# Performance work log

Measured on AMD Instinct MI355X. Metric: run time of the kernel, lower is better.

The kernel has to match this reference:

```python
import jax, jax.numpy as jnp
import numpy as np

B, S, D, F, E, K = 4, 1024, 512, 1024, 8, 2
LB_W, Z_W = 0.01, 0.001

def setup_inputs() -> dict:
    key = jax.random.key(0)
    k1, k2, k3, k4, k5 = jax.random.split(key, 5)
    std = 0.02
    x = jax.random.normal(k1, (B, S, D), dtype=jnp.float32)
    router_w = jax.random.normal(k2, (E, D), dtype=jnp.float32) * std  # nn.Linear weight [out,in]
    gate_w = jax.random.normal(k3, (E, D, F), dtype=jnp.float32) * std
    up_w = jax.random.normal(k4, (E, D, F), dtype=jnp.float32) * std
    down_w = jax.random.normal(k5, (E, F, D), dtype=jnp.float32) * std
    return {"x": x, "router_w": router_w, "gate_w": gate_w, "up_w": up_w, "down_w": down_w}

def reference(x, router_w, gate_w, up_w, down_w):
    b, s, d = x.shape
    e = router_w.shape[0]
    xf = x.reshape(-1, d)                      # [T, D]
    T = xf.shape[0]
    logits = xf @ router_w.T                   # [T, E]
    probs = jax.nn.softmax(logits, axis=-1)
    top_v, top_i = jax.lax.top_k(probs, K)     # [T, K]
    top_v = top_v / jnp.sum(top_v, axis=-1, keepdims=True)
    # combine[t, e] = sum_k top_v[t,k] * [top_i[t,k] == e]  (matches index_add_ accumulation)
    combine = jnp.zeros((T, e), dtype=xf.dtype).at[jnp.arange(T)[:, None], top_i].add(top_v)
    # SwiGLU experts, dense over E with weighted combine (same math as gather/scatter path)
    h_gate = jnp.einsum('td,edf->etf', xf, gate_w)   # [E, T, F]
    h_up = jnp.einsum('td,edf->etf', xf, up_w)       # [E, T, F]
    hidden = jax.nn.silu(h_gate) * h_up
    out = jnp.einsum('etf,efd,te->td', hidden, down_w, combine)  # [T, D]
    # auxiliary losses
    expert_mask = jax.nn.one_hot(top_i, e, dtype=jnp.float32).sum(axis=1)  # [T, E]
    f = expert_mask.sum(axis=0) / (T * K)
    P = probs.mean(axis=0)
    load_balance_loss = e * jnp.sum(f * P)
    z_loss = jnp.mean(jnp.square(jax.scipy.special.logsumexp(logits, axis=-1)))
    aux_loss = LB_W * load_balance_loss + Z_W * z_loss
    return out.reshape(b, s, d), aux_loss
```

## Files before the change

kernel.cpp:

```cpp
#include <hip/hip_runtime.h>

#define T_TOK 4096
#define D_DIM 512
#define F_DIM 1024
#define E_NUM 8
#define CAP   2048
#define BM    128
#define BN    64
#define BK    64
#define MT    (CAP/BM)
#define NT_GU (F_DIM/BN)
#define NT_DN (D_DIM/BN)
#define RB_TOK 32
#define CSTRIDE 32
#define RTR_BLOCKS (T_TOK/RB_TOK)

#define GU_HALF (BM*BK*2 + 2*BN*BK*2)
#define DN_HALF (BM*BK*2 + BN*BK*2)

typedef __bf16 bf16x8 __attribute__((ext_vector_type(8)));
typedef float  f32x4  __attribute__((ext_vector_type(4)));

__device__ __forceinline__ unsigned short f2bf(float f){
  unsigned int u = __builtin_bit_cast(unsigned int, f);
  u += 0x7FFFu + ((u >> 16) & 1u);
  return (unsigned short)(u >> 16);
}

__device__ __forceinline__ void gload16(const void* g, void* l){
  __builtin_amdgcn_global_load_lds(
      (const __attribute__((address_space(1))) unsigned int*)g,
      (__attribute__((address_space(3))) unsigned int*)l, 16, 0, 0);
}

__global__ __launch_bounds__(256) void prep_kernel(
    const float* __restrict__ x, const float* __restrict__ rw,
    const float* __restrict__ gw, const float* __restrict__ uw, const float* __restrict__ dw,
    unsigned short* __restrict__ Xg,
    unsigned short* __restrict__ gwt, unsigned short* __restrict__ uwt, unsigned short* __restrict__ dwt,
    int* __restrict__ cnt, int* __restrict__ slot_token, float* __restrict__ slot_w,
    float* __restrict__ Psum, float* __restrict__ zsum)
{
  __shared__ __align__(16) char smem[18432];
  int b = blockIdx.x;
  int tid = threadIdx.x;

  if (b >= RTR_BLOCKS){
    int tb = b - RTR_BLOCKS;
    int seg = tb >> 10;
    int r1023 = tb & 1023;
    int e = r1023 >> 7;
    int rr = r1023 & 127;
    const float* in; unsigned short* outp; int R, C, nbx;
    if (seg == 0){ in = gw; outp = gwt; R = D_DIM; C = F_DIM; nbx = F_DIM/64; }
    else if (seg == 1){ in = uw; outp = uwt; R = D_DIM; C = F_DIM; nbx = F_DIM/64; }
    else { in = dw; outp = dwt; R = F_DIM; C = D_DIM; nbx = D_DIM/64; }
    int c0 = (rr % nbx)*64, r0 = (rr / nbx)*64;
    const float* src = in + (size_t)e*R*C;
    unsigned short* dst = outp + (size_t)e*R*C;
    unsigned short* tile = (unsigned short*)smem;

    #pragma unroll
    for (int i=0;i<4;i++){
      int idx = i*256+tid;
      int rl = idx >> 4;
      int cseg = idx & 15;
      float4 v = *(const float4*)(src + (size_t)(r0+rl)*C + c0 + cseg*4);
      tile[(cseg*4+0)*68 + rl] = f2bf(v.x);
      tile[(cseg*4+1)*68 + rl] = f2bf(v.y);
      tile[(cseg*4+2)*68 + rl] = f2bf(v.z);
      tile[(cseg*4+3)*68 + rl] = f2bf(v.w);
    }
    __syncthreads();
    #pragma unroll
    for (int i=0;i<2;i++){
      int idx = i*256+tid;
      int c = idx >> 3;
      int rseg = idx & 7;
      ushort4 a = *(ushort4*)&tile[c*68 + rseg*8];
      ushort4 bq = *(ushort4*)&tile[c*68 + rseg*8 + 4];
      uint4 o;
      o.x = (unsigned)a.x  | ((unsigned)a.y<<16);
      o.y = (unsigned)a.z  | ((unsigned)a.w<<16);
      o.z = (unsigned)bq.x | ((unsigned)bq.y<<16);
      o.w = (unsigned)bq.z | ((unsigned)bq.w<<16);
      *(uint4*)(dst + (size_t)(c0+c)*R + r0 + rseg*8) = o;
    }
    return;
  }

  float* rws          = (float*)smem;
  float (*lp)[E_NUM]  = (float(*)[E_NUM])(smem+16384);
  float* lw1          = (float*)(smem+17408);
  float* lw2          = (float*)(smem+17536);
  float* llse         = (float*)(smem+17664);
  int*   li1          = (int*)(smem+17792);
  int*   li2          = (int*)(smem+17920);
  int*   lsl1         = (int*)(smem+18048);
  int*   lsl2         = (int*)(smem+18176);

  int wid = tid>>6, lane = tid&63;
  for (int i = tid; i < E_NUM*D_DIM; i += 256) rws[i] = rw[i];
  __syncthreads();

  uint4 pk[8];
  #pragma unroll
  for (int i=0;i<8;i++){
    int widx = wid*8 + i;
    int t = b*RB_TOK + widx;
    const float* xr = x + (size_t)t*D_DIM + lane*8;
    float4 xa = *(const float4*)xr;
    float4 xc = *(const float4*)(xr+4);
    pk[i].x = (unsigned)f2bf(xa.x) | ((unsigned)f2bf(xa.y)<<16);
    pk[i].y = (unsigned)f2bf(xa.z) | ((unsigned)f2bf(xa.w)<<16);
    pk[i].z = (unsigned)f2bf(xc.x) | ((unsigned)f2bf(xc.y)<<16);
    pk[i].w = (unsigned)f2bf(xc.z) | ((unsigned)f2bf(xc.w)<<16);

    float logit[E_NUM];
    #pragma unroll
    for (int e=0;e<E_NUM;e++){
      const float* wr = rws + e*D_DIM + lane*8;
      float4 wa = *(const float4*)wr;
      float4 wb = *(const float4*)(wr+4);
      float s = xa.x*wa.x + xa.y*wa.y + xa.z*wa.z + xa.w*wa.w
              + xc.x*wb.x + xc.y*wb.y + xc.z*wb.z + xc.w*wb.w;
      #pragma unroll
      for (int m=1;m<64;m<<=1) s += __shfl_xor(s, m);
      logit[e] = s;
    }
    float mx = logit[0];
    #pragma unroll
    for (int e=1;e<E_NUM;e++) mx = fmaxf(mx, logit[e]);
    float p[E_NUM]; float s = 0.f;
    #pragma unroll
    for (int e=0;e<E_NUM;e++){ p[e] = __expf(logit[e]-mx); s += p[e]; }
    float inv = 1.f/s;
    #pragma unroll
    for (int e=0;e<E_NUM;e++) p[e] *= inv;
    float lse = mx + __logf(s);
    int i1 = 0;
    #pragma unroll
    for (int e=1;e<E_NUM;e++) if (logit[e] > logit[i1]) i1 = e;
    int i2 = (i1==0) ? 1 : 0;
    #pragma unroll
    for (int e=0;e<E_NUM;e++) if (e != i1 && logit[e] > logit[i2]) i2 = e;
    if (lane == 0){
      float v1 = p[i1], v2 = p[i2];
      float invw = 1.f/(v1+v2);
      li1[widx] = i1; li2[widx] = i2;
      lw1[widx] = v1*invw; lw2[widx] = v2*invw;
      llse[widx] = lse;
      #pragma unroll
      for (int e=0;e<E_NUM;e++) lp[widx][e] = p[e];
    }
  }
  __syncthreads();

  if (tid < E_NUM){
    int e = tid, c = 0;
    #pragma unroll 4
    for (int j=0;j<RB_TOK;j++) c += (li1[j]==e) + (li2[j]==e);
    int idx = atomicAdd(&cnt[e*CSTRIDE], c);
    int tbase = b*RB_TOK;
    for (int j=0;j<RB_TOK;j++){
      if (li1[j]==e){ slot_token[e*CAP+idx] = tbase+j; slot_w[e*CAP+idx] = lw1[j]; lsl1[j] = e*CAP+idx; idx++; }
      if (li2[j]==e){ slot_token[e*CAP+idx] = tbase+j; slot_w[e*CAP+idx] = lw2[j]; lsl2[j] = e*CAP+idx; idx++; }
    }
    float ps = 0.f;
    #pragma unroll 4
    for (int j=0;j<RB_TOK;j++) ps += lp[j][e];
    atomicAdd(&Psum[e*CSTRIDE], ps);
  } else if (tid == 64){
    float zs = 0.f;
    #pragma unroll 4
    for (int j=0;j<RB_TOK;j++){ float l = llse[j]; zs += l*l; }
    atomicAdd(zsum, zs);
  }
  __syncthreads();

  #pragma unroll
  for (int i=0;i<8;i++){
    int widx = wid*8 + i;
    int s1 = lsl1[widx], s2 = lsl2[widx];
    *(uint4*)((char*)Xg + (size_t)s1*(D_DIM*2) + lane*16) = pk[i];
    *(uint4*)((char*)Xg + (size_t)s2*(D_DIM*2) + lane*16) = pk[i];
  }
}

__global__ __launch_bounds__(256) void gemm_gateup(
    const unsigned short* __restrict__ Xg, const unsigned short* __restrict__ gwt,
    const unsigned short* __restrict__ uwt,
    const int* __restrict__ cnt,
    const float* __restrict__ slot_w, unsigned short* __restrict__ H)
{
  int fid = blockIdx.x;
  int nid = (fid & 7)*(E_NUM*MT*NT_GU/8) + (fid >> 3);
  int e  = nid >> 8;
  int r  = nid & 255;
  int n0 = (r >> 4) * BN;
  int mt = r & 15;
  int c = cnt[e*CSTRIDE];
  int row0 = mt*BM;
  if (row0 >= c) return;
  int rem = c - row0;
  int offe = 0;
  #pragma unroll
  for (int i=0;i<E_NUM;i++) offe += (i < e) ? cnt[i*CSTRIDE] : 0;
  int tid = threadIdx.x, wid = tid>>6, lane = tid&63;
  __shared__ __align__(16) char arena[2*GU_HALF];

  int sub = lane>>3;
  int skb = ((lane&7)<<4) ^ (sub<<4);
  const char* asrc[4];
  #pragma unroll
  for (int i=0;i<4;i++){
    int rr = (wid*4+i)*8 + sub;
    asrc[i] = (const char*)Xg + ((size_t)e*CAP + row0 + rr)*(D_DIM*2) + skb;
  }
  const char* bgsrc[2]; const char* busrc[2];
  #pragma unroll
  for (int i=0;i<2;i++){
    int rr = (wid*2+i)*8 + sub;
    size_t rowb = ((size_t)e*F_DIM + n0 + rr) * (D_DIM*2);
    bgsrc[i] = (const char*)gwt + rowb + skb;
    busrc[i] = (const char*)uwt + rowb + skb;
  }

  f32x4 accg[4][2] = {};
  f32x4 accu[4][2] = {};
  int wm = wid>>1, wn = wid&1;

  auto STAGE = [&](int buf, int kt){
    size_t ko = (size_t)kt*BK*2;
    char* base = arena + buf*GU_HALF;
    #pragma unroll
    for (int i=0;i<4;i++)
      gload16(asrc[i]+ko, base + (wid*4+i)*1024);
    #pragma unroll
    for (int i=0;i<2;i++){
      gload16(bgsrc[i]+ko, base + BM*BK*2 + (wid*2+i)*1024);
      gload16(busrc[i]+ko, base + BM*BK*2 + BN*BK*2 + (wid*2+i)*1024);
    }
  };
  auto COMPUTE = [&](int buf){
    const char* base = arena + buf*GU_HALF;
    const char* Bg = base + BM*BK*2;
    const char* Bu = base + BM*BK*2 + BN*BK*2;
    #pragma unroll
    for (int s=0;s<2;s++){
      int kc = s*4 + (lane>>4);
      bf16x8 a[4], bg[2], bu[2];
      #pragma unroll
      for (int m=0;m<4;m++){
        int ar = wm*64 + m*16 + (lane&15);
        a[m] = *(const bf16x8*)(base + ar*128 + ((kc<<4) ^ ((ar&7)<<4)));
      }
      #pragma unroll
      for (int n=0;n<2;n++){
        int br = wn*32 + n*16 + (lane&15);
        int bo = br*128 + ((kc<<4) ^ ((br&7)<<4));
        bg[n] = *(const bf16x8*)(Bg + bo);
        bu[n] = *(const bf16x8*)(Bu + bo);
      }
      #pragma unroll
      for (int m=0;m<4;m++){
        #pragma unroll
        for (int n=0;n<2;n++){
          accg[m][n] = __builtin_amdgcn_mfma_f32_16x16x32_bf16(a[m], bg[n], accg[m][n], 0,0,0);
          accu[m][n] = __builtin_amdgcn_mfma_f32_16x16x32_bf16(a[m], bu[n], accu[m][n], 0,0,0);
        }
      }
    }
  };

  STAGE(0, 0);
  STAGE(1, 1);
  #pragma unroll 1
  for (int t=0; t<D_DIM/BK-1; ++t){
    asm volatile("s_waitcnt vmcnt(8)" ::: "memory");
    __builtin_amdgcn_s_barrier();
    __builtin_amdgcn_sched_barrier(0);
    COMPUTE(t & 1);
    __builtin_amdgcn_s_barrier();
    __builtin_amdgcn_sched_barrier(0);
    if (t+2 < D_DIM/BK) STAGE(t & 1, t+2);
  }
  asm volatile("s_waitcnt vmcnt(0)" ::: "memory");
  __builtin_amdgcn_s_barrier();
  __builtin_amdgcn_sched_barrier(0);
  COMPUTE((D_DIM/BK-1) & 1);

  #pragma unroll
  for (int m=0;m<4;m++){
    #pragma unroll
    for (int j=0;j<4;j++){
      int row = wm*64 + m*16 + ((lane>>4)<<2) + j;
      if (row < rem){
        float wgt = slot_w[e*CAP + row0 + row];
        size_t hb = (size_t)(offe + row0 + row)*F_DIM;
        #pragma unroll
        for (int n=0;n<2;n++){
          int col = n0 + wn*32 + n*16 + (lane&15);
          float g = accg[m][n][j];
          float u = accu[m][n][j];
          float h = g * (1.f/(1.f+__expf(-g))) * u * wgt;
          H[hb + col] = f2bf(h);
        }
      }
    }
  }
}

__global__ __launch_bounds__(256) void gemm_down(
    const unsigned short* __restrict__ H, const unsigned short* __restrict__ dwt,
    const int* __restrict__ cnt,
    const int* __restrict__ slot_token, float* __restrict__ out,
    const float* __restrict__ Psum, const float* __restrict__ zsum)
{
  int fid = blockIdx.x;
  int tid = threadIdx.x;
  if (fid == 0 && tid == 0){
    float lb = 0.f;
    #pragma unroll
    for (int e=0;e<E_NUM;e++){
      float f = (float)cnt[e*CSTRIDE] / (float)(T_TOK*2);
      float P = Psum[e*CSTRIDE] / (float)T_TOK;
      lb += f*P;
    }
    float z = zsum[0] / (float)T_TOK;
    out[(size_t)T_TOK*D_DIM] = 0.01f * ((float)E_NUM * lb) + 0.001f * z;
  }
  int nid = (fid & 7)*(E_NUM*MT*NT_DN/8) + (fid >> 3);
  int e  = nid >> 7;
  int r  = nid & 127;
  int n0 = (r >> 4) * BN;
  int mt = r & 15;
  int c = cnt[e*CSTRIDE];
  int row0 = mt*BM;
  if (row0 >= c) return;
  int rem = c - row0;
  int offe = 0;
  #pragma unroll
  for (int i=0;i<E_NUM;i++) offe += (i < e) ? cnt[i*CSTRIDE] : 0;
  int wid = tid>>6, lane = tid&63;
  __shared__ __align__(16) char arena[2*DN_HALF];
  int sub = lane>>3;
  int skb = ((lane&7)<<4) ^ (sub<<4);
  const char* asrc[4];
  #pragma unroll
  for (int i=0;i<4;i++){
    int rr = (wid*4+i)*8 + sub;
    asrc[i] = (const char*)H + ((size_t)offe + row0 + rr)*(F_DIM*2) + skb;
  }
  const char* bsrc[2];
  #pragma unroll
  for (int i=0;i<2;i++){
    int rr = (wid*2+i)*8 + sub;
    bsrc[i] = (const char*)dwt + ((size_t)e*D_DIM + n0 + rr)*(F_DIM*2) + skb;
  }
  f32x4 acc[4][2] = {};
  int wm = wid>>1, wn = wid&1;

  auto STAGE = [&](int buf, int kt){
    size_t ko = (size_t)kt*BK*2;
    char* base = arena + buf*DN_HALF;
    #pragma unroll
    for (int i=0;i<4;i++) gload16(asrc[i]+ko, base + (wid*4+i)*1024);
    #pragma unroll
    for (int i=0;i<2;i++) gload16(bsrc[i]+ko, base + BM*BK*2 + (wid*2+i)*1024);
  };
  auto COMPUTE = [&](int buf){
    const char* base = arena + buf*DN_HALF;
    const char* Bs = base + BM*BK*2;
    #pragma unroll
    for (int s=0;s<2;s++){
      int kc = s*4 + (lane>>4);
      bf16x8 a[4], bb[2];
      #pragma unroll
      for (int m=0;m<4;m++){
        int ar = wm*64 + m*16 + (lane&15);
        a[m] = *(const bf16x8*)(base + ar*128 + ((kc<<4) ^ ((ar&7)<<4)));
      }
      #pragma unroll
      for (int n=0;n<2;n++){
        int br = wn*32 + n*16 + (lane&15);
        bb[n] = *(const bf16x8*)(Bs + br*128 + ((kc<<4) ^ ((br&7)<<4)));
      }
      #pragma unroll
      for (int m=0;m<4;m++){
        #pragma unroll
        for (int n=0;n<2;n++)
          acc[m][n] = __builtin_amdgcn_mfma_f32_16x16x32_bf16(a[m], bb[n], acc[m][n], 0,0,0);
      }
    }
  };

  STAGE(0, 0);
  STAGE(1, 1);
  #pragma unroll 1
  for (int t=0; t<F_DIM/BK-1; ++t){
    asm volatile("s_waitcnt vmcnt(6)" ::: "memory");
    __builtin_amdgcn_s_barrier();
    __builtin_amdgcn_sched_barrier(0);
    COMPUTE(t & 1);
    __builtin_amdgcn_s_barrier();
    __builtin_amdgcn_sched_barrier(0);
    if (t+2 < F_DIM/BK) STAGE(t & 1, t+2);
  }
  asm volatile("s_waitcnt vmcnt(0)" ::: "memory");
  __builtin_amdgcn_s_barrier();
  __builtin_amdgcn_sched_barrier(0);
  COMPUTE((F_DIM/BK-1) & 1);

  #pragma unroll
  for (int m=0;m<4;m++){
    #pragma unroll
    for (int j=0;j<4;j++){
      int row = wm*64 + m*16 + ((lane>>4)<<2) + j;
      if (row < rem){
        int tok = slot_token[e*CAP + row0 + row];
        #pragma unroll
        for (int n=0;n<2;n++){
          int col = n0 + wn*32 + n*16 + (lane&15);
          atomicAdd(&out[(size_t)tok*D_DIM + col], acc[m][n][j]);
        }
      }
    }
  }
}

extern "C" void kernel_launch(void* const* d_in, const int* in_sizes, int n_in,
                              void* d_out, int out_size, void* d_ws, size_t ws_size,
                              hipStream_t stream){
  const float* x  = (const float*)d_in[0];
  const float* rw = (const float*)d_in[1];
  const float* gw = (const float*)d_in[2];
  const float* uw = (const float*)d_in[3];
  const float* dw = (const float*)d_in[4];
  float* out = (float*)d_out;

  char* w = (char*)d_ws;
  unsigned short* Xg  = (unsigned short*)w;  w += (size_t)E_NUM*CAP*D_DIM*2;
  unsigned short* gwt = (unsigned short*)w;  w += (size_t)E_NUM*D_DIM*F_DIM*2;
  unsigned short* uwt = (unsigned short*)w;  w += (size_t)E_NUM*D_DIM*F_DIM*2;
  unsigned short* dwt = (unsigned short*)w;  w += (size_t)E_NUM*F_DIM*D_DIM*2;
  unsigned short* H   = (unsigned short*)w;  w += (size_t)(T_TOK*2 + BM)*F_DIM*2;
  int*   slot_token = (int*)w;               w += (size_t)E_NUM*CAP*4;
  float* slot_w     = (float*)w;             w += (size_t)E_NUM*CAP*4;
  char* meta = w;
  int*   cnt  = (int*)w;       w += E_NUM*CSTRIDE*4;
  float* Psum = (float*)w;     w += E_NUM*CSTRIDE*4;
  float* zsum = (float*)w;     w += 128;
  size_t meta_bytes = (size_t)(w - meta);

  (void)hipMemsetAsync(d_out, 0, (size_t)out_size*sizeof(float), stream);
  (void)hipMemsetAsync(meta, 0, meta_bytes, stream);

  prep_kernel<<<RTR_BLOCKS + 3*1024, 256, 0, stream>>>(
      x, rw, gw, uw, dw, Xg, gwt, uwt, dwt, cnt, slot_token, slot_w, Psum, zsum);
  gemm_gateup<<<E_NUM*MT*NT_GU, 256, 0, stream>>>(Xg, gwt, uwt, cnt, slot_w, H);
  gemm_down<<<E_NUM*MT*NT_DN, 256, 0, stream>>>(H, dwt, cnt, slot_token, out, Psum, zsum);
}
```

Measured before the change: 200.0 us.

## Split prep into router and transpose kernels with packed swizzled LDS transpose

Splits the combined prep kernel into a separate router kernel and a dedicated weight transpose kernel. The transpose now loads two source rows per thread and packs them into 32-bit bf16 pairs. It stages them in an XOR-swizzled LDS tile so the transposed output is written as 32-byte contiguous chunks instead of scattered 16-bit LDS writes. This targets LDS bank conflicts and narrow shared-memory accesses, and lets the router use a smaller LDS footprint. The cost is one extra kernel launch and the loss of overlap between routing and transposition within a single grid.

```diff
diff --git a/kernel.cpp b/kernel.cpp
--- a/kernel.cpp
+++ b/kernel.cpp
@@ -13,7 +13,6 @@
 #define NT_DN (D_DIM/BN)
 #define RB_TOK 32
 #define CSTRIDE 32
-#define RTR_BLOCKS (T_TOK/RB_TOK)
 
 #define GU_HALF (BM*BK*2 + 2*BN*BK*2)
 #define DN_HALF (BM*BK*2 + BN*BK*2)
@@ -26,79 +25,26 @@
   u += 0x7FFFu + ((u >> 16) & 1u);
   return (unsigned short)(u >> 16);
 }
-
+__device__ __forceinline__ unsigned pk2(float a, float b){
+  return (unsigned)f2bf(a) | ((unsigned)f2bf(b)<<16);
+}
 __device__ __forceinline__ void gload16(const void* g, void* l){
   __builtin_amdgcn_global_load_lds(
       (const __attribute__((address_space(1))) unsigned int*)g,
       (__attribute__((address_space(3))) unsigned int*)l, 16, 0, 0);
 }
 
-__global__ __launch_bounds__(256) void prep_kernel(
+__global__ __launch_bounds__(256) void router_kernel(
     const float* __restrict__ x, const float* __restrict__ rw,
-    const float* __restrict__ gw, const float* __restrict__ uw, const float* __restrict__ dw,
     unsigned short* __restrict__ Xg,
-    unsigned short* __restrict__ gwt, unsigned short* __restrict__ uwt, unsigned short* __restrict__ dwt,
     int* __restrict__ cnt, int* __restrict__ slot_token, float* __restrict__ slot_w,
     float* __restrict__ Psum, float* __restrict__ zsum)
 {
-  __shared__ __align__(16) char smem[18432];
-  int b = blockIdx.x;
-  int tid = threadIdx.x;
-
-  if (b >= RTR_BLOCKS){
-    int tb = b - RTR_BLOCKS;
-    int seg = tb >> 10;
-    int r1023 = tb & 1023;
-    int e = r1023 >> 7;
-    int rr = r1023 & 127;
-    const float* in; unsigned short* outp; int R, C, nbx;
-    if (seg == 0){ in = gw; outp = gwt; R = D_DIM; C = F_DIM; nbx = F_DIM/64; }
-    else if (seg == 1){ in = uw; outp = uwt; R = D_DIM; C = F_DIM; nbx = F_DIM/64; }
-    else { in = dw; outp = dwt; R = F_DIM; C = D_DIM; nbx = D_DIM/64; }
-    int c0 = (rr % nbx)*64, r0 = (rr / nbx)*64;
-    const float* src = in + (size_t)e*R*C;
-    unsigned short* dst = outp + (size_t)e*R*C;
-    unsigned short* tile = (unsigned short*)smem;
-
-    #pragma unroll
-    for (int i=0;i<4;i++){
-      int idx = i*256+tid;
-      int rl = idx >> 4;
-      int cseg = idx & 15;
-      float4 v = *(const float4*)(src + (size_t)(r0+rl)*C + c0 + cseg*4);
-      tile[(cseg*4+0)*68 + rl] = f2bf(v.x);
-      tile[(cseg*4+1)*68 + rl] = f2bf(v.y);
-      tile[(cseg*4+2)*68 + rl] = f2bf(v.z);
-      tile[(cseg*4+3)*68 + rl] = f2bf(v.w);
-    }
-    __syncthreads();
-    #pragma unroll
-    for (int i=0;i<2;i++){
-      int idx = i*256+tid;
-      int c = idx >> 3;
-      int rseg = idx & 7;
-      ushort4 a = *(ushort4*)&tile[c*68 + rseg*8];
-      ushort4 bq = *(ushort4*)&tile[c*68 + rseg*8 + 4];
-      uint4 o;
-      o.x = (unsigned)a.x  | ((unsigned)a.y<<16);
-      o.y = (unsigned)a.z  | ((unsigned)a.w<<16);
-      o.z = (unsigned)bq.x | ((unsigned)bq.y<<16);
-      o.w = (unsigned)bq.z | ((unsigned)bq.w<<16);
-      *(uint4*)(dst + (size_t)(c0+c)*R + r0 + rseg*8) = o;
-    }
-    return;
-  }
-
-  float* rws          = (float*)smem;
-  float (*lp)[E_NUM]  = (float(*)[E_NUM])(smem+16384);
-  float* lw1          = (float*)(smem+17408);
-  float* lw2          = (float*)(smem+17536);
-  float* llse         = (float*)(smem+17664);
-  int*   li1          = (int*)(smem+17792);
-  int*   li2          = (int*)(smem+17920);
-  int*   lsl1         = (int*)(smem+18048);
-  int*   lsl2         = (int*)(smem+18176);
-
+  __shared__ float rws[E_NUM*D_DIM];
+  __shared__ float lp[RB_TOK][E_NUM];
+  __shared__ float lw1[RB_TOK], lw2[RB_TOK], llse[RB_TOK];
+  __shared__ int   li1[RB_TOK], li2[RB_TOK], lsl1[RB_TOK], lsl2[RB_TOK];
+  int b = blockIdx.x, tid = threadIdx.x;
   int wid = tid>>6, lane = tid&63;
   for (int i = tid; i < E_NUM*D_DIM; i += 256) rws[i] = rw[i];
   __syncthreads();
@@ -111,10 +57,10 @@
     const float* xr = x + (size_t)t*D_DIM + lane*8;
     float4 xa = *(const float4*)xr;
     float4 xc = *(const float4*)(xr+4);
-    pk[i].x = (unsigned)f2bf(xa.x) | ((unsigned)f2bf(xa.y)<<16);
-    pk[i].y = (unsigned)f2bf(xa.z) | ((unsigned)f2bf(xa.w)<<16);
-    pk[i].z = (unsigned)f2bf(xc.x) | ((unsigned)f2bf(xc.y)<<16);
-    pk[i].w = (unsigned)f2bf(xc.z) | ((unsigned)f2bf(xc.w)<<16);
+    pk[i].x = pk2(xa.x, xa.y);
+    pk[i].y = pk2(xa.z, xa.w);
+    pk[i].z = pk2(xc.x, xc.y);
+    pk[i].w = pk2(xc.z, xc.w);
 
     float logit[E_NUM];
     #pragma unroll
@@ -181,10 +127,53 @@
   #pragma unroll
   for (int i=0;i<8;i++){
     int widx = wid*8 + i;
-    int s1 = lsl1[widx], s2 = lsl2[widx];
-    *(uint4*)((char*)Xg + (size_t)s1*(D_DIM*2) + lane*16) = pk[i];
-    *(uint4*)((char*)Xg + (size_t)s2*(D_DIM*2) + lane*16) = pk[i];
-  }
+    *(uint4*)((char*)Xg + (size_t)lsl1[widx]*(D_DIM*2) + lane*16) = pk[i];
+    *(uint4*)((char*)Xg + (size_t)lsl2[widx]*(D_DIM*2) + lane*16) = pk[i];
+  }
+}
+
+__global__ __launch_bounds__(256) void transpose_kernel(
+    const float* __restrict__ gw, const float* __restrict__ uw, const float* __restrict__ dw,
+    unsigned short* __restrict__ gwt, unsigned short* __restrict__ uwt, unsigned short* __restrict__ dwt)
+{
+  __shared__ unsigned tw[64*32];
+  int tb = blockIdx.x;
+  int seg = tb >> 10;
+  int r1023 = tb & 1023;
+  int e = r1023 >> 7;
+  int rr = r1023 & 127;
+  const float* in; unsigned short* outp; int R, C, nbx;
+  if (seg == 0){ in = gw; outp = gwt; R = D_DIM; C = F_DIM; nbx = F_DIM/64; }
+  else if (seg == 1){ in = uw; outp = uwt; R = D_DIM; C = F_DIM; nbx = F_DIM/64; }
+  else { in = dw; outp = dwt; R = F_DIM; C = D_DIM; nbx = D_DIM/64; }
+  int c0 = (rr % nbx)*64, r0 = (rr / nbx)*64;
+  const float* src = in + (size_t)e*R*C;
+  unsigned short* dst = outp + (size_t)e*R*C;
+  int tid = threadIdx.x;
+
+  int d2 = tid>>3, fcq = tid&7;
+  const float* p0 = src + (size_t)(r0 + 2*d2)*C + c0 + fcq*8;
+  float4 a0 = *(const float4*)p0;
+  float4 a1 = *(const float4*)(p0+4);
+  float4 b0 = *(const float4*)(p0+C);
+  float4 b1 = *(const float4*)(p0+C+4);
+  float al[8] = {a0.x,a0.y,a0.z,a0.w,a1.x,a1.y,a1.z,a1.w};
+  float bl[8] = {b0.x,b0.y,b0.z,b0.w,b1.x,b1.y,b1.z,b1.w};
+  unsigned xb = ((unsigned)fcq)<<2;
+  #pragma unroll
+  for (int j=0;j<8;j++){
+    int c = fcq*8 + j;
+    tw[c*32 + (d2 ^ xb)] = pk2(al[j], bl[j]);
+  }
+  __syncthreads();
+
+  int c = tid>>2, q = tid&3;
+  unsigned xc = ((unsigned)(c>>3))<<2;
+  uint4 v0 = *(const uint4*)&tw[c*32 + ((unsigned)(q*8+0) ^ xc)];
+  uint4 v1 = *(const uint4*)&tw[c*32 + ((unsigned)(q*8+4) ^ xc)];
+  unsigned short* dp = dst + (size_t)(c0+c)*R + r0 + q*16;
+  *(uint4*)dp = v0;
+  *(uint4*)(dp+8) = v1;
 }
 
 __global__ __launch_bounds__(256) void gemm_gateup(
@@ -456,8 +445,9 @@
   (void)hipMemsetAsync(d_out, 0, (size_t)out_size*sizeof(float), stream);
   (void)hipMemsetAsync(meta, 0, meta_bytes, stream);
 
-  prep_kernel<<<RTR_BLOCKS + 3*1024, 256, 0, stream>>>(
-      x, rw, gw, uw, dw, Xg, gwt, uwt, dwt, cnt, slot_token, slot_w, Psum, zsum);
+  router_kernel<<<T_TOK/RB_TOK, 256, 0, stream>>>(
+      x, rw, Xg, cnt, slot_token, slot_w, Psum, zsum);
+  transpose_kernel<<<3*1024, 256, 0, stream>>>(gw, uw, dw, gwt, uwt, dwt);
   gemm_gateup<<<E_NUM*MT*NT_GU, 256, 0, stream>>>(Xg, gwt, uwt, cnt, slot_w, H);
   gemm_down<<<E_NUM*MT*NT_DN, 256, 0, stream>>>(H, dwt, cnt, slot_token, out, Psum, zsum);
 }
```

After: 209.5 us. +4.7%, slower.
